# Performance work log

Hardware: AMD Instinct MI355X
Metric: run time of the kernel (lower is better)

Reference implementation:

```python
import jax, jax.numpy as jnp
import numpy as np

B, S, D_MODEL = 8, 1024, 1024
N_HEADS, N_KV_HEADS, HEAD_DIM = 16, 8, 64
ROPE_THETA = 10000.0
LN_EPS = 1e-12


def setup_inputs() -> dict:
    key = jax.random.key(0)
    ks = jax.random.split(key, 6)
    sc = 0.02
    return {
        "hidden_states": jax.random.normal(ks[0], (B, S, D_MODEL), jnp.float32),
        "Wq": jax.random.normal(ks[1], (D_MODEL, N_HEADS * HEAD_DIM), jnp.float32) * sc,
        "bq": jnp.zeros((N_HEADS * HEAD_DIM,), jnp.float32),
        "Wk": jax.random.normal(ks[2], (D_MODEL, N_KV_HEADS * HEAD_DIM), jnp.float32) * sc,
        "bk": jnp.zeros((N_KV_HEADS * HEAD_DIM,), jnp.float32),
        "Wv": jax.random.normal(ks[3], (D_MODEL, N_KV_HEADS * HEAD_DIM), jnp.float32) * sc,
        "bv": jnp.zeros((N_KV_HEADS * HEAD_DIM,), jnp.float32),
        "Wo": jax.random.normal(ks[4], (N_HEADS * HEAD_DIM, D_MODEL), jnp.float32) * sc,
        "bo": jnp.zeros((D_MODEL,), jnp.float32),
        "ln_gamma": jnp.ones((D_MODEL,), jnp.float32),
        "ln_beta": jnp.zeros((D_MODEL,), jnp.float32),
    }


def _rope_tables(seq_len, dim, dtype):
    # lucidrains RotaryEmbedding: inv_freq over even indices, interleaved pairs
    inv_freq = 1.0 / (ROPE_THETA ** (jnp.arange(0, dim, 2, dtype=jnp.float32) / dim))
    angles = jnp.arange(seq_len, dtype=jnp.float32)[:, None] * inv_freq[None, :]  # [S, dim/2]
    return jnp.cos(angles).astype(dtype), jnp.sin(angles).astype(dtype)


def _apply_rope(x, cos, sin):
    # x: [B, S, H, D]; rotate interleaved pairs (x0,x1),(x2,x3),...
    x1 = x[..., 0::2]
    x2 = x[..., 1::2]
    c = cos[None, :, None, :]
    s = sin[None, :, None, :]
    y1 = x1 * c - x2 * s
    y2 = x1 * s + x2 * c
    return jnp.stack([y1, y2], axis=-1).reshape(x.shape)


def reference(hidden_states, Wq, bq, Wk, bk, Wv, bv, Wo, bo, ln_gamma, ln_beta):
    b, s, _ = hidden_states.shape
    q = (hidden_states @ Wq + bq).reshape(b, s, N_HEADS, HEAD_DIM)
    k = (hidden_states @ Wk + bk).reshape(b, s, N_KV_HEADS, HEAD_DIM)
    v = (hidden_states @ Wv + bv).reshape(b, s, N_KV_HEADS, HEAD_DIM)

    cos, sin = _rope_tables(s, HEAD_DIM, hidden_states.dtype)
    q = _apply_rope(q, cos, sin)
    k = _apply_rope(k, cos, sin)

    # GQA: repeat_interleave kv heads to match query heads (factor 2)
    rep = N_HEADS // N_KV_HEADS
    k = jnp.repeat(k, rep, axis=2)  # [B, S, H, D]
    v = jnp.repeat(v, rep, axis=2)

    scale = 1.0 / jnp.sqrt(jnp.asarray(HEAD_DIM, hidden_states.dtype))
    scores = jnp.einsum('bqhd,bkhd->bhqk', q * scale, k)  # [B, H, S, S]
    probs = jax.nn.softmax(scores, axis=-1)
    attn = jnp.einsum('bhqk,bkhd->bqhd', probs, v).reshape(b, s, N_HEADS * HEAD_DIM)

    out = attn @ Wo + bo
    resid = out + hidden_states
    mu = jnp.mean(resid, axis=-1, keepdims=True)
    var = jnp.mean(jnp.square(resid - mu), axis=-1, keepdims=True)
    normed = (resid - mu) * jax.lax.rsqrt(var + LN_EPS)
    return normed * ln_gamma + ln_beta
```

## Files before the change

kernel.cpp:

```cpp
#include <hip/hip_runtime.h>
#include <math.h>
#include <stdint.h>

typedef unsigned short u16;
typedef __bf16 bf16x8 __attribute__((ext_vector_type(8)));
typedef float f32x4 __attribute__((ext_vector_type(4)));

typedef const __attribute__((address_space(1))) void gv_t;
typedef __attribute__((address_space(3))) void lv_t;

__device__ __forceinline__ u16 f2bf(float f) {
    unsigned u = __builtin_bit_cast(unsigned, f);
    return (u16)((u + 0x7FFFu + ((u >> 16) & 1u)) >> 16);
}
__device__ __forceinline__ float bf2f(u16 h) {
    return __builtin_bit_cast(float, (unsigned)h << 16);
}
__device__ __forceinline__ void gll16(const void* g, void* l) {
    __builtin_amdgcn_global_load_lds((gv_t*)(uintptr_t)g,
                                     (lv_t*)(unsigned)(uintptr_t)l, 16, 0, 0);
}

__global__ __launch_bounds__(256) void cvt_bf16_kernel(
    const float* __restrict__ in, u16* __restrict__ out, int n4)
{
    int i = blockIdx.x * 256 + threadIdx.x;
    if (i >= n4) return;
    float4 f = ((const float4*)in)[i];
    ushort4 o = make_ushort4(f2bf(f.x), f2bf(f.y), f2bf(f.z), f2bf(f.w));
    ((ushort4*)out)[i] = o;
}

__global__ __launch_bounds__(256) void cvt_t4_kernel(
    const float* __restrict__ w0, const float* __restrict__ w1,
    const float* __restrict__ w2, const float* __restrict__ w3,
    u16* __restrict__ o0, u16* __restrict__ o1,
    u16* __restrict__ o2, u16* __restrict__ o3)
{
    __shared__ u16 t[64][65];
    const float* in; u16* out; int N;
    switch (blockIdx.z) {
        case 0: in = w0; out = o0; N = 1024; break;
        case 1: in = w1; out = o1; N = 512;  break;
        case 2: in = w2; out = o2; N = 512;  break;
        default: in = w3; out = o3; N = 1024; break;
    }
    int kb = blockIdx.y * 64, nb = blockIdx.x * 64;
    if (nb >= N) return;
    int tid = threadIdx.x;
#pragma unroll
    for (int c = 0; c < 16; ++c) {
        int id = c * 256 + tid;
        int r = id >> 6, n = id & 63;
        t[n][r] = f2bf(in[(size_t)(kb + r) * N + nb + n]);
    }
    __syncthreads();
#pragma unroll
    for (int c = 0; c < 16; ++c) {
        int id = c * 256 + tid;
        int r = id >> 6, n = id & 63;
        out[(size_t)(nb + r) * 1024 + kb + n] = t[r][n];
    }
}

template<int MODE>
__global__ __launch_bounds__(256) void gemm_mfma(
    const u16* __restrict__ A, const u16* __restrict__ Bt,
    const float* __restrict__ b0, const float* __restrict__ b1,
    const float* __restrict__ b2,
    const float* __restrict__ resid, float* __restrict__ Cf,
    u16* __restrict__ Qo, u16* __restrict__ Ko, u16* __restrict__ Vto,
    int N, int K)
{
    __shared__ __align__(16) u16 Asl[128 * 64];
    __shared__ __align__(16) u16 Bsl[128 * 64];
    const int tid = threadIdx.x, lane = tid & 63, w = tid >> 6;
    const int quad = lane >> 4, l16 = lane & 15;
    const int bm = blockIdx.y * 128, bn = blockIdx.x * 128;
    const int wm = (w >> 1) * 64, wn = (w & 1) * 64;

    f32x4 acc[4][4] = {};

    const int dr = lane >> 3;
    const int dcs = (((lane & 7) ^ dr) << 3);
    const u16* Ag = &A[(size_t)(bm + w * 32 + dr) * K + dcs];
    const u16* Bg = &Bt[(size_t)(bn + w * 32 + dr) * K + dcs];
    u16* Al = &Asl[(w * 32) * 64];
    u16* Bl = &Bsl[(w * 32) * 64];

    const int sw = l16 & 7;

    for (int k0 = 0; k0 < K; k0 += 64) {
#pragma unroll
        for (int c = 0; c < 4; ++c) {
            gll16(Ag + (size_t)(c * 8) * K + k0, Al + c * 8 * 64);
            gll16(Bg + (size_t)(c * 8) * K + k0, Bl + c * 8 * 64);
        }
        __syncthreads();
        bf16x8 af[4][2], bfr[4][2];
#pragma unroll
        for (int i = 0; i < 4; ++i)
#pragma unroll
            for (int ks = 0; ks < 2; ++ks)
                af[i][ks] = *(const bf16x8*)&Asl[(wm + i * 16 + l16) * 64 + (((ks * 4 + quad) ^ sw) << 3)];
#pragma unroll
        for (int j = 0; j < 4; ++j)
#pragma unroll
            for (int ks = 0; ks < 2; ++ks)
                bfr[j][ks] = *(const bf16x8*)&Bsl[(wn + j * 16 + l16) * 64 + (((ks * 4 + quad) ^ sw) << 3)];
#pragma unroll
        for (int i = 0; i < 4; ++i)
#pragma unroll
            for (int j = 0; j < 4; ++j)
#pragma unroll
                for (int ks = 0; ks < 2; ++ks)
                    acc[i][j] = __builtin_amdgcn_mfma_f32_16x16x32_bf16(af[i][ks], bfr[j][ks], acc[i][j], 0, 0, 0);
        __syncthreads();
    }

#pragma unroll
    for (int j = 0; j < 4; ++j) {
        int col = bn + wn + j * 16 + l16;
        if (MODE == 1) {
            float bb = b0[col];
#pragma unroll
            for (int i = 0; i < 4; ++i) {
                int row0 = bm + wm + i * 16 + quad * 4;
#pragma unroll
                for (int r = 0; r < 4; ++r) {
                    size_t off = (size_t)(row0 + r) * N + col;
                    Cf[off] = acc[i][j][r] + bb + resid[off];
                }
            }
        } else if (col < 1024) {
            float bb = b0[col];
#pragma unroll
            for (int i = 0; i < 4; ++i) {
                int row0 = bm + wm + i * 16 + quad * 4;
#pragma unroll
                for (int r = 0; r < 4; ++r)
                    Qo[(size_t)(row0 + r) * 1024 + col] = f2bf(acc[i][j][r] + bb);
            }
        } else if (col < 1536) {
            int c2 = col - 1024;
            float bb = b1[c2];
#pragma unroll
            for (int i = 0; i < 4; ++i) {
                int row0 = bm + wm + i * 16 + quad * 4;
#pragma unroll
                for (int r = 0; r < 4; ++r)
                    Ko[(size_t)(row0 + r) * 512 + c2] = f2bf(acc[i][j][r] + bb);
            }
        } else {
            int c2 = col - 1536, kvh = c2 >> 6, d = c2 & 63;
            float bb = b2[c2];
#pragma unroll
            for (int i = 0; i < 4; ++i) {
                int row0 = bm + wm + i * 16 + quad * 4;
                int b = row0 >> 10, s = row0 & 1023;
                ushort4 o4;
                o4.x = f2bf(acc[i][j][0] + bb);
                o4.y = f2bf(acc[i][j][1] + bb);
                o4.z = f2bf(acc[i][j][2] + bb);
                o4.w = f2bf(acc[i][j][3] + bb);
                *(ushort4*)&Vto[(size_t)((b * 8 + kvh) * 64 + d) * 1024 + s] = o4;
            }
        }
    }
}

__global__ __launch_bounds__(256) void rope_bf16_kernel(
    u16* __restrict__ x, int shift, int stride, int total)
{
    int idx = blockIdx.x * 256 + threadIdx.x;
    if (idx >= total) return;
    int j = idx & 31;
    int h = (idx >> 5) & ((1 << shift) - 1);
    int row = idx >> (5 + shift);
    int pos = row & 1023;
    float inv = exp2f((float)j * -0.4152410118609203f);
    float sn, cs;
    sincosf((float)pos * inv, &sn, &cs);
    unsigned* p = (unsigned*)&x[(size_t)row * stride + h * 64 + (j << 1)];
    unsigned u = *p;
    float x1 = bf2f((u16)(u & 0xffff)), x2 = bf2f((u16)(u >> 16));
    float y1 = x1 * cs - x2 * sn, y2 = x1 * sn + x2 * cs;
    *p = (unsigned)f2bf(y1) | ((unsigned)f2bf(y2) << 16);
}

__global__ __launch_bounds__(256) void attn_mfma(
    const u16* __restrict__ Q, const u16* __restrict__ K,
    const u16* __restrict__ Vt, u16* __restrict__ O)
{
    __shared__ __align__(16) u16 Ks[2][64 * 64];
    __shared__ __align__(16) u16 Vts[2][64 * 64];
    __shared__ __align__(16) u16 Ps[128][40];

    const int tid = threadIdx.x, lane = tid & 63, w = tid >> 6;
    const int quad = lane >> 4, l16 = lane & 15;
    const int qt = blockIdx.x, h = blockIdx.y, b = blockIdx.z;
    const int kvh = h >> 1;
    const size_t qrow0 = (size_t)b * 1024 + qt * 128;
    const size_t krow0 = (size_t)b * 1024;
    const u16* Vg = Vt + (size_t)((b * 8 + kvh) * 64) * 1024;

    const int dr = lane >> 3;
    const int dcs = (((lane & 7) ^ dr) << 3);
    const u16* Kg0 = &K[(krow0 + w * 16 + dr) * 512 + kvh * 64 + dcs];
    const u16* Vg0 = &Vg[(size_t)(w * 16 + dr) * 1024 + dcs];
    const int sw = l16 & 7;
    const float C1 = 0.18033688011112043f;

#pragma unroll
    for (int c = 0; c < 2; ++c) {
        gll16(Kg0 + (size_t)(c * 8) * 512, &Ks[0][(w * 16 + c * 8) * 64]);
        gll16(Vg0 + (size_t)(c * 8) * 1024, &Vts[0][(w * 16 + c * 8) * 64]);
    }

    bf16x8 qf[2][2];
#pragma unroll
    for (int qg = 0; qg < 2; ++qg) {
        int qrow = w * 32 + qg * 16 + l16;
        float fpos = (float)(qt * 128 + qrow);
#pragma unroll
        for (int ks = 0; ks < 2; ++ks) {
            uint4 qraw = *(const uint4*)&Q[(qrow0 + qrow) * 1024 + h * 64 + ks * 32 + quad * 8];
            unsigned o_[4];
#pragma unroll
            for (int t = 0; t < 4; ++t) {
                int j = ks * 16 + quad * 4 + t;
                float inv = exp2f((float)j * -0.4152410118609203f);
                float sn_, cs_;
                sincosf(fpos * inv, &sn_, &cs_);
                cs_ *= C1; sn_ *= C1;
                unsigned u = (&qraw.x)[t];
                float x1 = bf2f((u16)(u & 0xffff)), x2 = bf2f((u16)(u >> 16));
                float y1 = x1 * cs_ - x2 * sn_, y2 = x1 * sn_ + x2 * cs_;
                o_[t] = (unsigned)f2bf(y1) | ((unsigned)f2bf(y2) << 16);
            }
            qf[qg][ks] = __builtin_bit_cast(bf16x8, make_uint4(o_[0], o_[1], o_[2], o_[3]));
        }
    }

    f32x4 acc_o[2][4] = {};
    f32x4 lsum[2] = {};
    const bf16x8 ones = __builtin_bit_cast(bf16x8,
        make_uint4(0x3F803F80u, 0x3F803F80u, 0x3F803F80u, 0x3F803F80u));

    for (int kt = 0; kt < 16; ++kt) {
        const int cur = kt & 1;
        __syncthreads();

        if (kt < 15) {
#pragma unroll
            for (int c = 0; c < 2; ++c) {
                gll16(Kg0 + (size_t)((kt + 1) * 64 + c * 8) * 512,
                      &Ks[cur ^ 1][(w * 16 + c * 8) * 64]);
                gll16(Vg0 + (size_t)(c * 8) * 1024 + (kt + 1) * 64,
                      &Vts[cur ^ 1][(w * 16 + c * 8) * 64]);
            }
        }

        f32x4 s[2][4] = {};
#pragma unroll
        for (int ks = 0; ks < 2; ++ks) {
#pragma unroll
            for (int nt = 0; nt < 4; ++nt) {
                bf16x8 ak = *(const bf16x8*)&Ks[cur][(nt * 16 + l16) * 64 + (((ks * 4 + quad) ^ sw) << 3)];
                s[0][nt] = __builtin_amdgcn_mfma_f32_16x16x32_bf16(ak, qf[0][ks], s[0][nt], 0, 0, 0);
                s[1][nt] = __builtin_amdgcn_mfma_f32_16x16x32_bf16(ak, qf[1][ks], s[1][nt], 0, 0, 0);
            }
        }

#pragma unroll
        for (int kc = 0; kc < 2; ++kc) {
#pragma unroll
            for (int qg = 0; qg < 2; ++qg) {
#pragma unroll
                for (int ntl = 0; ntl < 2; ++ntl) {
                    int nt = kc * 2 + ntl;
                    float p0 = __builtin_amdgcn_exp2f(s[qg][nt][0]);
                    float p1 = __builtin_amdgcn_exp2f(s[qg][nt][1]);
                    unsigned pk0 = __builtin_amdgcn_perm(
                        __builtin_bit_cast(unsigned, p1),
                        __builtin_bit_cast(unsigned, p0), 0x07060302u);
                    float p2 = __builtin_amdgcn_exp2f(s[qg][nt][2]);
                    float p3 = __builtin_amdgcn_exp2f(s[qg][nt][3]);
                    unsigned pk1 = __builtin_amdgcn_perm(
                        __builtin_bit_cast(unsigned, p3),
                        __builtin_bit_cast(unsigned, p2), 0x07060302u);
                    *(uint2*)&Ps[w * 32 + qg * 16 + l16][ntl * 16 + quad * 4] = make_uint2(pk0, pk1);
                }
            }
            bf16x8 bp0 = *(const bf16x8*)&Ps[w * 32 + l16][quad * 8];
            bf16x8 bp1 = *(const bf16x8*)&Ps[w * 32 + 16 + l16][quad * 8];
            lsum[0] = __builtin_amdgcn_mfma_f32_16x16x32_bf16(ones, bp0, lsum[0], 0, 0, 0);
            lsum[1] = __builtin_amdgcn_mfma_f32_16x16x32_bf16(ones, bp1, lsum[1], 0, 0, 0);
#pragma unroll
            for (int nt = 0; nt < 4; ++nt) {
                bf16x8 av = *(const bf16x8*)&Vts[cur][(nt * 16 + l16) * 64 + (((kc * 4 + quad) ^ sw) << 3)];
                acc_o[0][nt] = __builtin_amdgcn_mfma_f32_16x16x32_bf16(av, bp0, acc_o[0][nt], 0, 0, 0);
                acc_o[1][nt] = __builtin_amdgcn_mfma_f32_16x16x32_bf16(av, bp1, acc_o[1][nt], 0, 0, 0);
            }
        }
    }

#pragma unroll
    for (int qg = 0; qg < 2; ++qg) {
        float rl = 1.0f / lsum[qg][0];
        size_t orow = (qrow0 + w * 32 + qg * 16 + l16) * 1024 + h * 64;
#pragma unroll
        for (int nt = 0; nt < 4; ++nt) {
            ushort4 o4;
            o4.x = f2bf(acc_o[qg][nt][0] * rl);
            o4.y = f2bf(acc_o[qg][nt][1] * rl);
            o4.z = f2bf(acc_o[qg][nt][2] * rl);
            o4.w = f2bf(acc_o[qg][nt][3] * rl);
            *(ushort4*)&O[orow + nt * 16 + quad * 4] = o4;
        }
    }
}

__global__ __launch_bounds__(256) void ln_kernel(float* __restrict__ io,
    const float* __restrict__ gamma, const float* __restrict__ beta)
{
    int row = blockIdx.x;
    int tid = threadIdx.x;
    float* p = io + (size_t)row * 1024;
    float4 x = *reinterpret_cast<const float4*>(&p[tid << 2]);
    float s = x.x + x.y + x.z + x.w;
    float ss = fmaf(x.x, x.x, fmaf(x.y, x.y, fmaf(x.z, x.z, x.w * x.w)));
#pragma unroll
    for (int off = 32; off > 0; off >>= 1) {
        s  += __shfl_down(s, off);
        ss += __shfl_down(ss, off);
    }
    __shared__ float rs[4], rss[4];
    int lane = tid & 63, wid = tid >> 6;
    if (lane == 0) { rs[wid] = s; rss[wid] = ss; }
    __syncthreads();
    float S = rs[0] + rs[1] + rs[2] + rs[3];
    float SS = rss[0] + rss[1] + rss[2] + rss[3];
    float mu = S * (1.0f / 1024.0f);
    float var = SS * (1.0f / 1024.0f) - mu * mu;
    float rstd = rsqrtf(var + 1e-12f);
    float4 g = *reinterpret_cast<const float4*>(&gamma[tid << 2]);
    float4 be = *reinterpret_cast<const float4*>(&beta[tid << 2]);
    float4 o;
    o.x = (x.x - mu) * rstd * g.x + be.x;
    o.y = (x.y - mu) * rstd * g.y + be.y;
    o.z = (x.z - mu) * rstd * g.z + be.z;
    o.w = (x.w - mu) * rstd * g.w + be.w;
    *reinterpret_cast<float4*>(&p[tid << 2]) = o;
}

extern "C" void kernel_launch(void* const* d_in, const int* in_sizes, int n_in,
                              void* d_out, int out_size, void* d_ws, size_t ws_size,
                              hipStream_t stream)
{
    (void)in_sizes; (void)n_in; (void)out_size; (void)ws_size;
    const float* hidden = (const float*)d_in[0];
    const float* Wq = (const float*)d_in[1];
    const float* bq = (const float*)d_in[2];
    const float* Wk = (const float*)d_in[3];
    const float* bk = (const float*)d_in[4];
    const float* Wv = (const float*)d_in[5];
    const float* bv = (const float*)d_in[6];
    const float* Wo = (const float*)d_in[7];
    const float* bo = (const float*)d_in[8];
    const float* g  = (const float*)d_in[9];
    const float* be = (const float*)d_in[10];
    float* out = (float*)d_out;

    u16* hb  = (u16*)d_ws;
    u16* Wqt = hb  + (size_t)8192 * 1024;
    u16* Wkt = Wqt + (size_t)1024 * 1024;
    u16* Wvt = Wkt + (size_t)512 * 1024;
    u16* Wot = Wvt + (size_t)512 * 1024;
    u16* Qb  = Wot + (size_t)1024 * 1024;
    u16* Kb  = Qb  + (size_t)8192 * 1024;
    u16* Vtb = Kb  + (size_t)8192 * 512;

    cvt_bf16_kernel<<<8192, 256, 0, stream>>>(hidden, hb, 8192 * 1024 / 4);
    cvt_t4_kernel<<<dim3(16, 16, 4), 256, 0, stream>>>(Wq, Wk, Wv, Wo, Wqt, Wkt, Wvt, Wot);

    gemm_mfma<0><<<dim3(16, 64), 256, 0, stream>>>(hb, Wqt, bq, bk, bv,
        nullptr, nullptr, Qb, Kb, Vtb, 2048, 1024);

    rope_bf16_kernel<<<8192, 256, 0, stream>>>(Kb, 3, 512, 8192 * 8 * 32);

    attn_mfma<<<dim3(8, 16, 8), 256, 0, stream>>>(Qb, Kb, Vtb, Qb);

    gemm_mfma<1><<<dim3(8, 64), 256, 0, stream>>>(Qb, Wot, bo, nullptr, nullptr,
        hidden, out, nullptr, nullptr, nullptr, 1024, 1024);
    ln_kernel<<<8192, 256, 0, stream>>>(out, g, be);
}
```

Before: 261.0 us.

## Tune attention kernel occupancy, XCD-aware block order, and MFMA priority

The attention kernel now uses a 1D grid with a block-index remap. Consecutive blocks on the same XCD then share batch and head, so K/V stay in that L2. The P staging buffer is halved and reused per query group, V fragments are hoisted out of that loop, and launch bounds request 4 blocks per CU to raise occupancy. s_setprio brackets the MFMA sections to favour matrix issue. The risks are register pressure or spills from the occupancy hint, and more LDS round trips per query group.

```diff
diff --git a/kernel.cpp b/kernel.cpp
--- a/kernel.cpp
+++ b/kernel.cpp
@@ -188,17 +188,19 @@
     *p = (unsigned)f2bf(y1) | ((unsigned)f2bf(y2) << 16);
 }
 
-__global__ __launch_bounds__(256) void attn_mfma(
+__global__ __launch_bounds__(256, 4) void attn_mfma(
     const u16* __restrict__ Q, const u16* __restrict__ K,
     const u16* __restrict__ Vt, u16* __restrict__ O)
 {
     __shared__ __align__(16) u16 Ks[2][64 * 64];
     __shared__ __align__(16) u16 Vts[2][64 * 64];
-    __shared__ __align__(16) u16 Ps[128][40];
+    __shared__ __align__(16) u16 Ps[64][40];
 
     const int tid = threadIdx.x, lane = tid & 63, w = tid >> 6;
     const int quad = lane >> 4, l16 = lane & 15;
-    const int qt = blockIdx.x, h = blockIdx.y, b = blockIdx.z;
+    const int id = blockIdx.x;
+    const int nid = (id & 7) * 128 + (id >> 3);
+    const int qt = nid & 7, h = (nid >> 3) & 15, b = nid >> 7;
     const int kvh = h >> 1;
     const size_t qrow0 = (size_t)b * 1024 + qt * 128;
     const size_t krow0 = (size_t)b * 1024;
@@ -262,6 +264,7 @@
         }
 
         f32x4 s[2][4] = {};
+        __builtin_amdgcn_s_setprio(1);
 #pragma unroll
         for (int ks = 0; ks < 2; ++ks) {
 #pragma unroll
@@ -271,9 +274,14 @@
                 s[1][nt] = __builtin_amdgcn_mfma_f32_16x16x32_bf16(ak, qf[1][ks], s[1][nt], 0, 0, 0);
             }
         }
+        __builtin_amdgcn_s_setprio(0);
 
 #pragma unroll
         for (int kc = 0; kc < 2; ++kc) {
+            bf16x8 av[4];
+#pragma unroll
+            for (int nt = 0; nt < 4; ++nt)
+                av[nt] = *(const bf16x8*)&Vts[cur][(nt * 16 + l16) * 64 + (((kc * 4 + quad) ^ sw) << 3)];
 #pragma unroll
             for (int qg = 0; qg < 2; ++qg) {
 #pragma unroll
@@ -289,18 +297,15 @@
                     unsigned pk1 = __builtin_amdgcn_perm(
                         __builtin_bit_cast(unsigned, p3),
                         __builtin_bit_cast(unsigned, p2), 0x07060302u);
-                    *(uint2*)&Ps[w * 32 + qg * 16 + l16][ntl * 16 + quad * 4] = make_uint2(pk0, pk1);
+                    *(uint2*)&Ps[w * 16 + l16][ntl * 16 + quad * 4] = make_uint2(pk0, pk1);
                 }
-            }
-            bf16x8 bp0 = *(const bf16x8*)&Ps[w * 32 + l16][quad * 8];
-            bf16x8 bp1 = *(const bf16x8*)&Ps[w * 32 + 16 + l16][quad * 8];
-            lsum[0] = __builtin_amdgcn_mfma_f32_16x16x32_bf16(ones, bp0, lsum[0], 0, 0, 0);
-            lsum[1] = __builtin_amdgcn_mfma_f32_16x16x32_bf16(ones, bp1, lsum[1], 0, 0, 0);
-#pragma unroll
-            for (int nt = 0; nt < 4; ++nt) {
-                bf16x8 av = *(const bf16x8*)&Vts[cur][(nt * 16 + l16) * 64 + (((kc * 4 + quad) ^ sw) << 3)];
-                acc_o[0][nt] = __builtin_amdgcn_mfma_f32_16x16x32_bf16(av, bp0, acc_o[0][nt], 0, 0, 0);
-                acc_o[1][nt] = __builtin_amdgcn_mfma_f32_16x16x32_bf16(av, bp1, acc_o[1][nt], 0, 0, 0);
+                bf16x8 bp = *(const bf16x8*)&Ps[w * 16 + l16][quad * 8];
+                __builtin_amdgcn_s_setprio(1);
+                lsum[qg] = __builtin_amdgcn_mfma_f32_16x16x32_bf16(ones, bp, lsum[qg], 0, 0, 0);
+#pragma unroll
+                for (int nt = 0; nt < 4; ++nt)
+                    acc_o[qg][nt] = __builtin_amdgcn_mfma_f32_16x16x32_bf16(av[nt], bp, acc_o[qg][nt], 0, 0, 0);
+                __builtin_amdgcn_s_setprio(0);
             }
         }
     }
@@ -389,7 +394,7 @@
 
     rope_bf16_kernel<<<8192, 256, 0, stream>>>(Kb, 3, 512, 8192 * 8 * 32);
 
-    attn_mfma<<<dim3(8, 16, 8), 256, 0, stream>>>(Qb, Kb, Vtb, Qb);
+    attn_mfma<<<dim3(1024), 256, 0, stream>>>(Qb, Kb, Vtb, Qb);
 
     gemm_mfma<1><<<dim3(8, 64), 256, 0, stream>>>(Qb, Wot, bo, nullptr, nullptr,
         hidden, out, nullptr, nullptr, nullptr, 1024, 1024);
```

New measurement: 249.9 us. -4.2%, faster.
